# Kernel tuning notes

Hardware: AMD Instinct MI355X
Metric: run time of the kernel (lower is better)

Reference implementation:

```python
import jax, jax.numpy as jnp
import numpy as np

BLOCK_SIZE = 32       # MXFP block size (OCP microscaling spec)
E2M1_MAX = 6.0        # max magnitude representable in FP4 E2M1
E2M1_EMAX = 2.0       # exponent of max binade (4..6)


def quantize_mxfp4(t):
    """Fake-quantize t to MXFP4 (E2M1 elements, E8M0 shared scale) along last dim.

    Matches MXFP_F.extract_mxfp_components + dequant: per block of 32 values a
    power-of-two shared scale 2^(floor(log2(amax)) - emax_elem), elements
    rounded to nearest E2M1 value {0, +-0.5, 1, 1.5, 2, 3, 4, 6}.
    """
    shp = t.shape
    tb = t.reshape(shp[:-1] + (shp[-1] // BLOCK_SIZE, BLOCK_SIZE))
    amax = jnp.max(jnp.abs(tb), axis=-1, keepdims=True)
    safe_amax = jnp.where(amax > 0, amax, 1.0)
    shared_exp = jnp.floor(jnp.log2(safe_amax)) - E2M1_EMAX  # E8M0 exponent
    scale = jnp.exp2(shared_exp)
    v = tb / scale
    av = jnp.abs(v)
    # E2M1 grid spacing: 0.5 in [0,2), 1 in [2,4), 2 in [4,6]
    e = jnp.clip(jnp.floor(jnp.log2(jnp.maximum(av, 2.0 ** -10))), 0.0, E2M1_EMAX)
    step = jnp.exp2(e - 1.0)  # one mantissa bit
    q = jnp.clip(jnp.round(av / step) * step, 0.0, E2M1_MAX) * jnp.sign(v)
    return (q * scale).reshape(shp)


def setup_inputs() -> dict:
    key = jax.random.key(0)
    kx, kw, kb = jax.random.split(key, 3)
    B, S, K, N = 2, 4096, 4096, 4096
    x = jax.random.normal(kx, (B, S, K), dtype=jnp.float32)
    weight = jax.random.normal(kw, (N, K), dtype=jnp.float32) * 0.02
    bias = jax.random.normal(kb, (N,), dtype=jnp.float32) * 0.02
    return {"x": x, "weight": weight, "bias": bias}


def reference(x, weight, bias):
    # layer_type 'XqWqB': quantize activations (block along in_features) and
    # weights (block_dim=1 == in_features); bias stays full precision.
    xq = quantize_mxfp4(x)                 # [B, S, K]
    wq = quantize_mxfp4(weight)            # [N, K]
    out = jnp.einsum("bsk,nk->bsn", xq, wq) + bias
    return out
```

## Files before the change

kernel.cpp:

```cpp
#include <hip/hip_runtime.h>
#include <hip/hip_bf16.h>

typedef __attribute__((ext_vector_type(4))) int i32x4;
typedef __attribute__((ext_vector_type(8))) int i32x8;
typedef __attribute__((ext_vector_type(16))) float f32x16;

#define GLOBAL_CPTR(x) ((__attribute__((address_space(1))) const void*)(x))
#define LDS_PTR(x)     ((__attribute__((address_space(3))) void*)(x))

__global__ __launch_bounds__(256) void mxfp4_quant_pack_kernel(
    const float* __restrict__ xin, unsigned char* __restrict__ xq,
    unsigned char* __restrict__ xsc, const float* __restrict__ win,
    unsigned char* __restrict__ wq, unsigned char* __restrict__ wsc,
    int kshift, int gx) {
  const int KC = 1 << (kshift - 5);
  const int CQ = KC >> 2;
  const int bid0 = blockIdx.x;
  const float* in;
  unsigned char* outq;
  unsigned char* outsc;
  int bid;
  if (bid0 < gx) { in = xin; outq = xq; outsc = xsc; bid = bid0; }
  else           { in = win; outq = wq; outsc = wsc; bid = bid0 - gx; }

  const int cq  = bid & (CQ - 1);
  const int R   = (bid >> (kshift - 7)) << 6;
  const int t   = threadIdx.x;

  __shared__ float sf[64 * 132];

  const float* base = in + ((size_t)R << kshift) + (cq << 7);
#pragma unroll
  for (int i = 0; i < 8; ++i) {
    const int g   = i * 256 + t;
    const int row = g >> 5;
    const int c4  = g & 31;
    float4 v = *reinterpret_cast<const float4*>(
        base + ((size_t)row << kshift) + (c4 << 2));
    *reinterpret_cast<float4*>(sf + row * 132 + (c4 << 2)) = v;
  }
  __syncthreads();

  const int rl = (t & 3) + ((t >> 4) << 2);
  const int kc = (t >> 2) & 3;
  const float* src = sf + rl * 132 + (kc << 5);
  float v[32];
#pragma unroll
  for (int i = 0; i < 8; ++i)
    *reinterpret_cast<float4*>(v + 4 * i) =
        *reinterpret_cast<const float4*>(src + 4 * i);

  float am = 0.f;
#pragma unroll
  for (int j = 0; j < 32; ++j) am = fmaxf(am, fabsf(v[j]));

  const float safe = am > 0.f ? am : 1.f;
  const int se = ilogbf(safe) - 2;
  const float inv = ldexpf(1.f, -se);

  unsigned int packs[4] = {0, 0, 0, 0};
#pragma unroll
  for (int j = 0; j < 32; ++j) {
    const float val = v[j] * inv;
    const float av = fabsf(val);
    const float avc = fmaxf(av, 9.765625e-4f);
    int ee = (int)((__float_as_uint(avc) >> 23) & 0xFF) - 127;
    ee = ee < 0 ? 0 : (ee > 2 ? 2 : ee);
    const float istep = __uint_as_float((unsigned)(128 - ee) << 23);
    const int m = (int)rintf(av * istep);
    unsigned int c = (unsigned)(m + (ee << 1));
    c = c > 7u ? 7u : c;
    c |= (__float_as_uint(val) >> 28) & 8u;
    packs[j >> 3] |= c << (4 * (j & 7));
  }

  const int row = R + rl;
  const size_t chunk = (size_t)(row >> 8) * KC + (cq << 2) + kc;
  *reinterpret_cast<uint4*>(outq + chunk * 4096 + (size_t)(row & 255) * 16) =
      make_uint4(packs[0], packs[1], packs[2], packs[3]);
  outsc[chunk * 256 + (row & 31) * 8 + ((row >> 5) & 7)] =
      (unsigned char)(se + 127);
}

#define BM 256
#define BN 256
#define NTHR 512
#define BUFS 34816

__global__ __launch_bounds__(NTHR, 2) void mxfp_gemm_kernel(
    const unsigned char* __restrict__ Aq, const unsigned char* __restrict__ Asc,
    const unsigned char* __restrict__ Bq, const unsigned char* __restrict__ Bsc,
    const float* __restrict__ bias, float* __restrict__ C,
    int M, int N, int K) {
  __shared__ unsigned char lds[4 * BUFS];

  const int tid = threadIdx.x;
  const int l   = tid & 63;
  const int wid = tid >> 6;
  const int wm  = wid >> 2;
  const int wn  = wid & 3;

  const int nwg = gridDim.x;
  const int bid = blockIdx.x;
  const int swz = (bid & 7) * (nwg >> 3) + (bid >> 3);
  const int nbn = N / BN;
  const int bm  = swz / nbn;
  const int bn  = swz % nbn;

  const int KC = K >> 5;

  f32x16 acc[4][2] = {};

#define STAGE(BUFO, KT)                                                        \
  do {                                                                         \
    const int cl = wid & 3;                                                    \
    const int rg2 = (wid >> 2) << 1;                                           \
    const size_t abase = ((size_t)bm * KC + (size_t)(KT) * 4 + cl) * 4096;     \
    const size_t bbase = ((size_t)bn * KC + (size_t)(KT) * 4 + cl) * 4096;     \
    _Pragma("unroll") for (int i = 0; i < 2; ++i) {                            \
      __builtin_amdgcn_global_load_lds(                                        \
          GLOBAL_CPTR(Aq + abase + (rg2 + i) * 1024 + (l << 4)),               \
          LDS_PTR(lds + (BUFO) + cl * 4096 + (rg2 + i) * 1024), 16, 0, 0);     \
      __builtin_amdgcn_global_load_lds(                                        \
          GLOBAL_CPTR(Bq + bbase + (rg2 + i) * 1024 + (l << 4)),               \
          LDS_PTR(lds + (BUFO) + 16384 + cl * 4096 + (rg2 + i) * 1024),        \
          16, 0, 0);                                                           \
    }                                                                          \
    if (wid < 4) {                                                             \
      __builtin_amdgcn_global_load_lds(                                        \
          GLOBAL_CPTR(Asc + ((size_t)bm * KC + (size_t)(KT) * 4 + wid) * 256   \
                      + (l << 2)),                                             \
          LDS_PTR(lds + (BUFO) + 32768 + wid * 256), 4, 0, 0);                 \
    } else {                                                                   \
      __builtin_amdgcn_global_load_lds(                                        \
          GLOBAL_CPTR(Bsc + ((size_t)bn * KC + (size_t)(KT) * 4 + (wid - 4))   \
                      * 256 + (l << 2)),                                       \
          LDS_PTR(lds + (BUFO) + 33792 + (wid - 4) * 256), 4, 0, 0);           \
    }                                                                          \
  } while (0)

#define MFMA1(MB, NB, AV, BV)                                                  \
  acc[MB][NB] = __builtin_amdgcn_mfma_scale_f32_32x32x64_f8f6f4(               \
      a8[MB], b8[NB], acc[MB][NB], 4, 4, MB, AV, NB, BV)

#define KTILE(BUFO)                                                            \
  do {                                                                         \
    const i32x4 z4 = {0, 0, 0, 0};                                             \
    _Pragma("unroll") for (int ks = 0; ks < 2; ++ks) {                         \
      const int cofs = (ks << 13) + ((l & 32) << 7);    \
      i32x8 a8[4], b8[2];                                                      \
      _Pragma("unroll") for (int mb = 0; mb < 4; ++mb)                         \
        a8[mb] = __builtin_shufflevector(                                      \
            *(const i32x4*)(lds + (BUFO) + cofs +                              \
                            (((wm << 7) + (mb << 5) + (l & 31)) << 4)),        \
            z4, 0, 1, 2, 3, 4, 5, 6, 7);                                       \
      _Pragma("unroll") for (int nb = 0; nb < 2; ++nb)                         \
        b8[nb] = __builtin_shufflevector(                                      \
            *(const i32x4*)(lds + (BUFO) + 16384 + cofs +                      \
                            (((wn << 6) + (nb << 5) + (l & 31)) << 4)),        \
            z4, 0, 1, 2, 3, 4, 5, 6, 7);                                       \
      const int av = *(const int*)(lds + (BUFO) + 32768 + (cofs >> 4) +        \
                                   ((l & 31) << 3) + (wm << 2));               \
      const int bv = *(const ushort*)(lds + (BUFO) + 33792 + (cofs >> 4) +     \
                                      ((l & 31) << 3) + (wn << 1));            \
      MFMA1(0, 0, av, bv); MFMA1(0, 1, av, bv);                                \
      MFMA1(1, 0, av, bv); MFMA1(1, 1, av, bv);                                \
      MFMA1(2, 0, av, bv); MFMA1(2, 1, av, bv);                                \
      MFMA1(3, 0, av, bv); MFMA1(3, 1, av, bv);                                \
    }                                                                          \
  } while (0)

  STAGE(0, 0);
  STAGE(BUFS, 1);
  asm volatile("s_waitcnt vmcnt(0)" ::: "memory");
  __builtin_amdgcn_s_barrier();
  asm volatile("" ::: "memory");

  const int NKT = K >> 7;
  for (int w = 0; w < (NKT >> 1); ++w) {
    const int t = w << 1;
    const int c = (w & 1) ? 2 * BUFS : 0;
    const int p = (w & 1) ? 0 : 2 * BUFS;
    const int t2 = (t + 2 < NKT) ? (t + 2) : (NKT - 1);
    const int t3 = (t + 3 < NKT) ? (t + 3) : (NKT - 1);
    STAGE(p, t2);
    KTILE(c);
    STAGE(p + BUFS, t3);
    KTILE(c + BUFS);
    asm volatile("s_waitcnt vmcnt(0)" ::: "memory");
    __builtin_amdgcn_s_barrier();
    asm volatile("" ::: "memory");
  }

  const int colb = bn * BN + wn * 64 + (l & 31);
  const int rowb = bm * BM + wm * 128 + ((l >> 5) << 2);
  const float bv0 = bias[colb];
  const float bv1 = bias[colb + 32];
#pragma unroll
  for (int mb = 0; mb < 4; ++mb) {
#pragma unroll
    for (int nb = 0; nb < 2; ++nb) {
      const float bv = nb ? bv1 : bv0;
      const int col = colb + nb * 32;
#pragma unroll
      for (int r = 0; r < 16; ++r) {
        const int row = rowb + mb * 32 + ((r >> 2) << 3) + (r & 3);
        C[(size_t)row * N + col] = acc[mb][nb][r] + bv;
      }
    }
  }
}

extern "C" void kernel_launch(void* const* d_in, const int* in_sizes, int n_in,
                              void* d_out, int out_size, void* d_ws, size_t ws_size,
                              hipStream_t stream) {
  const float* x    = (const float*)d_in[0];
  const float* w    = (const float*)d_in[1];
  const float* bias = (const float*)d_in[2];
  float* out = (float*)d_out;

  const int N = in_sizes[2];
  const int K = in_sizes[1] / N;
  const int M = (int)((long long)in_sizes[0] / K);
  const int kshift = __builtin_ctz(K);

  unsigned char* xq  = (unsigned char*)d_ws;
  unsigned char* wq  = xq + ((size_t)M * K >> 1);
  unsigned char* xsc = wq + ((size_t)N * K >> 1);
  unsigned char* wsc = xsc + ((size_t)M * K >> 5);

  const int CQ = (K >> 5) >> 2;
  const int gx = (M >> 6) * CQ;
  const int gw = (N >> 6) * CQ;

  mxfp4_quant_pack_kernel<<<dim3((unsigned)(gx + gw)), dim3(256), 0, stream>>>(
      x, xq, xsc, w, wq, wsc, kshift, gx);

  dim3 grid((M / BM) * (N / BN));
  mxfp_gemm_kernel<<<grid, dim3(NTHR), 0, stream>>>(xq, xsc, wq, wsc, bias, out,
                                                    M, N, K);
}
```

Baseline: 136.8 us.

## Load B operand directly from global into registers, shrink LDS to double buffer

B-tile FP4 data is no longer staged through LDS. Each lane reads its B fragments straight from global memory into registers inside the k-tile loop, while A and both scale arrays stay in LDS. LDS use drops from four buffers to two, and the pipeline becomes a one-tile-ahead double buffer with a barrier every k-tile. This cuts LDS traffic and footprint, but it exposes global-load latency on B inside the compute loop, shortens prefetch depth, and adds twice as many barriers.

```diff
diff --git a/kernel.cpp b/kernel.cpp
--- a/kernel.cpp
+++ b/kernel.cpp
@@ -85,14 +85,14 @@
 #define BM 256
 #define BN 256
 #define NTHR 512
-#define BUFS 34816
+#define BUFS 18432
 
 __global__ __launch_bounds__(NTHR, 2) void mxfp_gemm_kernel(
     const unsigned char* __restrict__ Aq, const unsigned char* __restrict__ Asc,
     const unsigned char* __restrict__ Bq, const unsigned char* __restrict__ Bsc,
     const float* __restrict__ bias, float* __restrict__ C,
     int M, int N, int K) {
-  __shared__ unsigned char lds[4 * BUFS];
+  __shared__ unsigned char lds[2 * BUFS];
 
   const int tid = threadIdx.x;
   const int l   = tid & 63;
@@ -109,6 +109,10 @@
 
   const int KC = K >> 5;
 
+  const unsigned char* bLane = Bq + (((size_t)bn * KC) << 12) +
+                               ((size_t)(l >> 5) << 12) + (wn << 10) +
+                               ((l & 31) << 4);
+
   f32x16 acc[4][2] = {};
 
 #define STAGE(BUFO, KT)                                                        \
@@ -116,26 +120,21 @@
     const int cl = wid & 3;                                                    \
     const int rg2 = (wid >> 2) << 1;                                           \
     const size_t abase = ((size_t)bm * KC + (size_t)(KT) * 4 + cl) * 4096;     \
-    const size_t bbase = ((size_t)bn * KC + (size_t)(KT) * 4 + cl) * 4096;     \
     _Pragma("unroll") for (int i = 0; i < 2; ++i) {                            \
       __builtin_amdgcn_global_load_lds(                                        \
           GLOBAL_CPTR(Aq + abase + (rg2 + i) * 1024 + (l << 4)),               \
           LDS_PTR(lds + (BUFO) + cl * 4096 + (rg2 + i) * 1024), 16, 0, 0);     \
-      __builtin_amdgcn_global_load_lds(                                        \
-          GLOBAL_CPTR(Bq + bbase + (rg2 + i) * 1024 + (l << 4)),               \
-          LDS_PTR(lds + (BUFO) + 16384 + cl * 4096 + (rg2 + i) * 1024),        \
-          16, 0, 0);                                                           \
     }                                                                          \
     if (wid < 4) {                                                             \
       __builtin_amdgcn_global_load_lds(                                        \
           GLOBAL_CPTR(Asc + ((size_t)bm * KC + (size_t)(KT) * 4 + wid) * 256   \
                       + (l << 2)),                                             \
-          LDS_PTR(lds + (BUFO) + 32768 + wid * 256), 4, 0, 0);                 \
+          LDS_PTR(lds + (BUFO) + 16384 + wid * 256), 4, 0, 0);                 \
     } else {                                                                   \
       __builtin_amdgcn_global_load_lds(                                        \
           GLOBAL_CPTR(Bsc + ((size_t)bn * KC + (size_t)(KT) * 4 + (wid - 4))   \
                       * 256 + (l << 2)),                                       \
-          LDS_PTR(lds + (BUFO) + 33792 + (wid - 4) * 256), 4, 0, 0);           \
+          LDS_PTR(lds + (BUFO) + 17408 + (wid - 4) * 256), 4, 0, 0);           \
     }                                                                          \
   } while (0)
 
@@ -143,9 +142,15 @@
   acc[MB][NB] = __builtin_amdgcn_mfma_scale_f32_32x32x64_f8f6f4(               \
       a8[MB], b8[NB], acc[MB][NB], 4, 4, MB, AV, NB, BV)
 
-#define KTILE(BUFO)                                                            \
+#define KTILE(BUFO, KT)                                                        \
   do {                                                                         \
     const i32x4 z4 = {0, 0, 0, 0};                                             \
+    const unsigned char* bt = bLane + ((size_t)(KT) << 14);                    \
+    i32x4 braw[2][2];                                                          \
+    _Pragma("unroll") for (int ks = 0; ks < 2; ++ks)                           \
+      _Pragma("unroll") for (int nb = 0; nb < 2; ++nb)                         \
+        braw[ks][nb] =                                                         \
+            *(const i32x4*)(bt + (ks << 13) + (nb << 9));                      \
     _Pragma("unroll") for (int ks = 0; ks < 2; ++ks) {                         \
       const int cofs = (ks << 13) + ((l & 32) << 7);    \
       i32x8 a8[4], b8[2];                                                      \
@@ -155,13 +160,11 @@
                             (((wm << 7) + (mb << 5) + (l & 31)) << 4)),        \
             z4, 0, 1, 2, 3, 4, 5, 6, 7);                                       \
       _Pragma("unroll") for (int nb = 0; nb < 2; ++nb)                         \
-        b8[nb] = __builtin_shufflevector(                                      \
-            *(const i32x4*)(lds + (BUFO) + 16384 + cofs +                      \
-                            (((wn << 6) + (nb << 5) + (l & 31)) << 4)),        \
-            z4, 0, 1, 2, 3, 4, 5, 6, 7);                                       \
-      const int av = *(const int*)(lds + (BUFO) + 32768 + (cofs >> 4) +        \
+        b8[nb] = __builtin_shufflevector(braw[ks][nb], z4,                     \
+                                         0, 1, 2, 3, 4, 5, 6, 7);              \
+      const int av = *(const int*)(lds + (BUFO) + 16384 + (cofs >> 4) +        \
                                    ((l & 31) << 3) + (wm << 2));               \
-      const int bv = *(const ushort*)(lds + (BUFO) + 33792 + (cofs >> 4) +     \
+      const int bv = *(const ushort*)(lds + (BUFO) + 17408 + (cofs >> 4) +     \
                                       ((l & 31) << 3) + (wn << 1));            \
       MFMA1(0, 0, av, bv); MFMA1(0, 1, av, bv);                                \
       MFMA1(1, 0, av, bv); MFMA1(1, 1, av, bv);                                \
@@ -171,22 +174,17 @@
   } while (0)
 
   STAGE(0, 0);
-  STAGE(BUFS, 1);
   asm volatile("s_waitcnt vmcnt(0)" ::: "memory");
   __builtin_amdgcn_s_barrier();
   asm volatile("" ::: "memory");
 
   const int NKT = K >> 7;
-  for (int w = 0; w < (NKT >> 1); ++w) {
-    const int t = w << 1;
-    const int c = (w & 1) ? 2 * BUFS : 0;
-    const int p = (w & 1) ? 0 : 2 * BUFS;
-    const int t2 = (t + 2 < NKT) ? (t + 2) : (NKT - 1);
-    const int t3 = (t + 3 < NKT) ? (t + 3) : (NKT - 1);
-    STAGE(p, t2);
-    KTILE(c);
-    STAGE(p + BUFS, t3);
-    KTILE(c + BUFS);
+  for (int t = 0; t < NKT; ++t) {
+    const int tn = (t + 1 < NKT) ? (t + 1) : t;
+    const int bufC = (t & 1) ? BUFS : 0;
+    const int bufN = (t & 1) ? 0 : BUFS;
+    STAGE(bufN, tn);
+    KTILE(bufC, t);
     asm volatile("s_waitcnt vmcnt(0)" ::: "memory");
     __builtin_amdgcn_s_barrier();
     asm volatile("" ::: "memory");
```

After: 147.4 us. +7.7%, slower.
